# Kernel tuning notes

Measured on AMD Instinct MI355X. Metric: run time of the kernel, lower is better.

Reference implementation:

```python
import jax, jax.numpy as jnp
import numpy as np

B, H, W, C = 32, 112, 112, 96
HEADS, WS, SHIFT = 3, 7, 3
N = WS * WS            # tokens per window (49)
NW = (H // WS) * (W // WS)  # windows per image (256)
HD = C // HEADS


def _rel_pos_index():
    coords = np.stack(np.meshgrid(np.arange(WS), np.arange(WS), indexing='ij'))  # (2,ws,ws)
    cf = coords.reshape(2, -1)
    rel = (cf[:, :, None] - cf[:, None, :]).transpose(1, 2, 0)  # (N,N,2)
    rel[:, :, 0] += WS - 1
    rel[:, :, 1] += WS - 1
    rel[:, :, 0] *= 2 * WS - 1
    return jnp.asarray(rel.sum(-1))  # (N,N) int


def _attn_mask():
    img = np.zeros((H, W))
    sl = (slice(0, -WS), slice(-WS, -SHIFT), slice(-SHIFT, None))
    cnt = 0
    for hs in sl:
        for ws_ in sl:
            img[hs, ws_] = cnt
            cnt += 1
    mw = img.reshape(H // WS, WS, W // WS, WS).transpose(0, 2, 1, 3).reshape(-1, N)
    am = mw[:, None, :] - mw[:, :, None]
    return jnp.asarray(np.where(am != 0, -100.0, 0.0).astype(np.float32))  # (nW,N,N)


REL_IDX = _rel_pos_index()
ATTN_MASK = _attn_mask()


def _ln(x, w, b):
    m = x.mean(-1, keepdims=True)
    v = x.var(-1, keepdims=True)
    return (x - m) / jnp.sqrt(v + 1e-5) * w + b


def setup_inputs() -> dict:
    key = jax.random.key(0)
    ks = jax.random.split(key, 8)
    s = 0.02
    return {
        'x': jax.random.normal(ks[0], (B, H * W, C), jnp.float32),
        'norm1_w': jnp.ones((C,), jnp.float32),
        'norm1_b': jnp.zeros((C,), jnp.float32),
        'qkv_w': jax.random.normal(ks[1], (3 * C, C), jnp.float32) * s,
        'qkv_b': jnp.zeros((3 * C,), jnp.float32),
        'proj_w': jax.random.normal(ks[2], (C, C), jnp.float32) * s,
        'proj_b': jnp.zeros((C,), jnp.float32),
        'rpb_table': jax.random.normal(ks[3], ((2 * WS - 1) ** 2, HEADS), jnp.float32) * s,
        'norm2_w': jnp.ones((C,), jnp.float32),
        'norm2_b': jnp.zeros((C,), jnp.float32),
        'fc1_w': jax.random.normal(ks[4], (4 * C, C), jnp.float32) * s,
        'fc1_b': jnp.zeros((4 * C,), jnp.float32),
        'fc2_w': jax.random.normal(ks[5], (C, 4 * C), jnp.float32) * s,
        'fc2_b': jnp.zeros((C,), jnp.float32),
    }


def reference(x, norm1_w, norm1_b, qkv_w, qkv_b, proj_w, proj_b, rpb_table,
              norm2_w, norm2_b, fc1_w, fc1_b, fc2_w, fc2_b):
    shortcut = x
    xn = _ln(x, norm1_w, norm1_b).reshape(B, H, W, C)
    # cyclic shift
    xs = jnp.roll(xn, (-SHIFT, -SHIFT), axis=(1, 2))
    # window partition -> (B*nW, N, C)
    xw = xs.reshape(B, H // WS, WS, W // WS, WS, C).transpose(0, 1, 3, 2, 4, 5).reshape(B * NW, N, C)
    # windowed multi-head attention
    qkv = (xw @ qkv_w.T + qkv_b).reshape(B * NW, N, 3, HEADS, HD).transpose(2, 0, 3, 1, 4)
    q, k, v = qkv[0], qkv[1], qkv[2]
    attn = jnp.einsum('bhnd,bhmd->bhnm', q * (HD ** -0.5), k)
    bias = rpb_table[REL_IDX].transpose(2, 0, 1)  # (heads,N,N)
    attn = attn + bias[None]
    attn = attn.reshape(B, NW, HEADS, N, N) + ATTN_MASK[None, :, None]
    attn = jax.nn.softmax(attn.reshape(B * NW, HEADS, N, N), axis=-1)
    o = jnp.einsum('bhnm,bhmd->bhnd', attn, v).transpose(0, 2, 1, 3).reshape(B * NW, N, C)
    o = o @ proj_w.T + proj_b
    # window reverse + reverse shift
    xr = o.reshape(B, H // WS, W // WS, WS, WS, C).transpose(0, 1, 3, 2, 4, 5).reshape(B, H, W, C)
    xr = jnp.roll(xr, (SHIFT, SHIFT), axis=(1, 2)).reshape(B, H * W, C)
    # MLP (note: applied to norm2 of attention output, as in the source)
    xn2 = _ln(xr, norm2_w, norm2_b)
    h1 = jax.nn.gelu(xn2 @ fc1_w.T + fc1_b, approximate=False)
    mlp = h1 @ fc2_w.T + fc2_b
    return shortcut + xr + mlp
```

## Files before the change

### kernel.cpp

```cpp
#include <hip/hip_runtime.h>
#include <hip/hip_bf16.h>

#define NTOK 401408

typedef __attribute__((ext_vector_type(8))) short s8v;
typedef __attribute__((ext_vector_type(4))) float f4v;

__device__ __forceinline__ float bs2f(short s) {
  unsigned u = ((unsigned)(unsigned short)s) << 16;
  float f; __builtin_memcpy(&f, &u, 4); return f;
}
__device__ __forceinline__ short f2bs(float f) {
  __hip_bfloat16 b = __float2bfloat16(f);
  return *reinterpret_cast<short*>(&b);
}
__device__ __forceinline__ s8v ld8(const short* p) { return *(const s8v*)p; }
__device__ __forceinline__ int rgn(int a) { return (a < 105) ? 0 : ((a < 109) ? 1 : 2); }

__device__ __forceinline__ void wave_lds_fence() {
  asm volatile("s_waitcnt lgkmcnt(0)" ::: "memory");
  __builtin_amdgcn_sched_barrier(0);
}

__device__ __forceinline__ void ld8d(const void* base, size_t elem, int isb, float* o) {
  if (isb) {
    s8v v = *(const s8v*)((const short*)base + elem);
    #pragma unroll
    for (int j = 0; j < 8; j++) o[j] = bs2f(v[j]);
  } else {
    const float* f = (const float*)base + elem;
    float4 a = *(const float4*)f;
    float4 b = *(const float4*)(f + 4);
    o[0]=a.x; o[1]=a.y; o[2]=a.z; o[3]=a.w; o[4]=b.x; o[5]=b.y; o[6]=b.z; o[7]=b.w;
  }
}
__device__ __forceinline__ void st8d(void* base, size_t elem, int isb, const float* v) {
  if (isb) {
    s8v o;
    #pragma unroll
    for (int j = 0; j < 8; j++) o[j] = f2bs(v[j]);
    *(s8v*)((short*)base + elem) = o;
  } else {
    float* f = (float*)base + elem;
    float4 a = {v[0], v[1], v[2], v[3]};
    float4 b = {v[4], v[5], v[6], v[7]};
    *(float4*)f = a;
    *(float4*)(f + 4) = b;
  }
}
__device__ __forceinline__ float lddf(const void* base, size_t elem, int isb) {
  return isb ? bs2f(((const short*)base)[elem]) : ((const float*)base)[elem];
}
__device__ __forceinline__ void stdf(void* base, size_t elem, int isb, float v) {
  if (isb) ((short*)base)[elem] = f2bs(v); else ((float*)base)[elem] = v;
}

#define OQW   0
#define OQB   27648
#define OPW   27936
#define OPB   37152
#define ORPB  37248
#define ON1W  37760
#define ON1B  37856
#define ON2W  37952
#define ON2B  38048
#define OF1W  38144
#define OF1B  75008
#define OF2W  75392
#define OF2B  112256

__global__ __launch_bounds__(256) void k_detect_convert(
    const void* x,
    const void* qw, const void* qb, const void* pw, const void* pb, const void* rpb,
    const void* n1w, const void* n1b, const void* n2w, const void* n2b,
    const void* f1w, const void* f1b, const void* f2w, const void* f2b,
    int* flag, short* wb)
{
  __shared__ int cnt_sh;
  if (threadIdx.x == 0) cnt_sh = 0;
  __syncthreads();
  const unsigned* xw = (const unsigned*)x;
  int c = 0;
  for (int i = threadIdx.x; i < 1024; i += 256) {
    unsigned e = (xw[i] >> 7) & 0xFFu;
    if (e >= 0x70u && e <= 0x8Fu) c++;
  }
  atomicAdd(&cnt_sh, c);
  __syncthreads();
  const int isb = (cnt_sh > 512) ? 1 : 0;
  if (blockIdx.x == 0 && threadIdx.x == 0) *flag = isb;

  const void* srcs[13] = {qw, qb, pw, pb, rpb, n1w, n1b, n2w, n2b, f1w, f1b, f2w, f2b};
  const int   ns[13]   = {27648, 288, 9216, 96, 507, 96, 96, 96, 96, 36864, 384, 36864, 96};
  const int   offs[13] = {OQW, OQB, OPW, OPB, ORPB, ON1W, ON1B, ON2W, ON2B, OF1W, OF1B, OF2W, OF2B};
  const int gtid = blockIdx.x * 256 + threadIdx.x;
  for (int a = 0; a < 13; a++) {
    const void* s = srcs[a];
    for (int i = gtid; i < ns[a]; i += 64 * 256)
      wb[offs[a] + i] = f2bs(isb ? bs2f(((const short*)s)[i]) : ((const float*)s)[i]);
  }
}

__global__ __launch_bounds__(192, 3) void k_attn_fused(
    const void* __restrict__ xg, const short* __restrict__ wb,
    const int* __restrict__ flag, void* __restrict__ xrout)
{
  __shared__ __align__(16) short smem[22272];

  const int isb = *flag;
  const int h = threadIdx.x >> 6;
  const int lane = threadIdx.x & 63;
  const int quad = lane >> 4, l15 = lane & 15;
  const int wi = blockIdx.x;
  const int bb = wi >> 8, wp = wi & 255, wh = wp >> 4, ww = wp & 15;

  short* Qh = smem + h * 5120;
  short* Kh = Qh + 2560;
  short* Ph = smem + h * 5120;
  short* Vh = smem + 15360 + h * 2304;

  float gwv[3][8], gbv[3][8];
  #pragma unroll
  for (int kc = 0; kc < 3; kc++) {
    s8v g = ld8(wb + ON1W + kc * 32 + quad * 8);
    s8v t = ld8(wb + ON1B + kc * 32 + quad * 8);
    #pragma unroll
    for (int j = 0; j < 8; j++) { gwv[kc][j] = bs2f(g[j]); gbv[kc][j] = bs2f(t[j]); }
  }

  s8v af[4][3];
  #pragma unroll
  for (int rt = 0; rt < 4; rt++) {
    int n = rt * 16 + l15; if (n > 48) n = 48;
    int ii = n / 7, jj = n - ii * 7;
    int hi = wh * 7 + ii + 3; if (hi >= 112) hi -= 112;
    int wj = ww * 7 + jj + 3; if (wj >= 112) wj -= 112;
    size_t rowoff = ((size_t)bb * 12544 + hi * 112 + wj) * 96;
    float v[3][8]; float sm = 0.f, sq = 0.f;
    #pragma unroll
    for (int kc = 0; kc < 3; kc++) {
      ld8d(xg, rowoff + kc * 32 + quad * 8, isb, v[kc]);
      #pragma unroll
      for (int j = 0; j < 8; j++) { sm += v[kc][j]; sq += v[kc][j] * v[kc][j]; }
    }
    sm += __shfl_xor(sm, 16); sm += __shfl_xor(sm, 32);
    sq += __shfl_xor(sq, 16); sq += __shfl_xor(sq, 32);
    float mean = sm * (1.f / 96.f);
    float var  = sq * (1.f / 96.f) - mean * mean;
    float rstd = rsqrtf(var + 1e-5f);
    #pragma unroll
    for (int kc = 0; kc < 3; kc++) {
      s8v o;
      #pragma unroll
      for (int j = 0; j < 8; j++) o[j] = f2bs((v[kc][j] - mean) * rstd * gwv[kc][j] + gbv[kc][j]);
      af[rt][kc] = o;
    }
  }

  const float qscale = 0.1767766952966369f;
  #pragma unroll
  for (int s = 0; s < 3; s++) {
    #pragma unroll
    for (int nt = 0; nt < 2; nt++) {
      int col = s * 96 + h * 32 + nt * 16 + l15;
      const short* wrow = wb + OQW + (size_t)col * 96;
      s8v b0 = ld8(wrow + quad * 8), b1 = ld8(wrow + 32 + quad * 8), b2 = ld8(wrow + 64 + quad * 8);
      float bias = bs2f(wb[OQB + col]);
      #pragma unroll
      for (int rt = 0; rt < 4; rt++) {
        f4v acc = {0.f, 0.f, 0.f, 0.f};
        acc = __builtin_amdgcn_mfma_f32_16x16x32_bf16(af[rt][0], b0, acc, 0, 0, 0);
        acc = __builtin_amdgcn_mfma_f32_16x16x32_bf16(af[rt][1], b1, acc, 0, 0, 0);
        acc = __builtin_amdgcn_mfma_f32_16x16x32_bf16(af[rt][2], b2, acc, 0, 0, 0);
        #pragma unroll
        for (int r = 0; r < 4; r++) {
          int tok = rt * 16 + quad * 4 + r;
          float val = acc[r] + bias;
          int cc = nt * 16 + l15;
          if (s == 0)      Qh[tok * 40 + cc] = f2bs(val * qscale);
          else if (s == 1) Kh[tok * 40 + cc] = f2bs(val);
          else             Vh[cc * 72 + tok] = f2bs(val);
        }
      }
    }
  }
  wave_lds_fence();

  s8v qa[4], kb[4], vf[2][2];
  #pragma unroll
  for (int t = 0; t < 4; t++) {
    qa[t] = *(const s8v*)&Qh[(t * 16 + l15) * 40 + quad * 8];
    kb[t] = *(const s8v*)&Kh[(t * 16 + l15) * 40 + quad * 8];
  }
  #pragma unroll
  for (int nt = 0; nt < 2; nt++)
    #pragma unroll
    for (int kc = 0; kc < 2; kc++)
      vf[nt][kc] = *(const s8v*)&Vh[(nt * 16 + l15) * 72 + kc * 32 + quad * 8];

  int crid[4], ci[4], cj[4]; bool cv[4];
  #pragma unroll
  for (int nt = 0; nt < 4; nt++) {
    int col = nt * 16 + l15;
    cv[nt] = (col < 49);
    int ki = col / 7, kj = col - ki * 7;
    ci[nt] = ki; cj[nt] = kj;
    crid[nt] = rgn(wh * 7 + ki) * 3 + rgn(ww * 7 + kj);
  }

  #pragma unroll
  for (int rt = 0; rt < 4; rt++) {
    f4v sc4[4];
    #pragma unroll
    for (int nt = 0; nt < 4; nt++) {
      f4v z = {0.f, 0.f, 0.f, 0.f};
      sc4[nt] = __builtin_amdgcn_mfma_f32_16x16x32_bf16(qa[rt], kb[nt], z, 0, 0, 0);
    }
    #pragma unroll
    for (int rr = 0; rr < 4; rr++) {
      int row = rt * 16 + quad * 4 + rr;
      bool vr = (row < 49);
      int ri = row / 7, rj = row - ri * 7;
      int rrid = rgn(wh * 7 + ri) * 3 + rgn(ww * 7 + rj);
      float vals[4];
      float m = -1e30f;
      #pragma unroll
      for (int nt = 0; nt < 4; nt++) {
        float sv;
        if (vr && cv[nt]) {
          int bidx = (ri - ci[nt] + 6) * 13 + (rj - cj[nt] + 6);
          float bias = bs2f(wb[ORPB + bidx * 3 + h]);
          sv = sc4[nt][rr] + bias + ((rrid == crid[nt]) ? 0.f : -100.f);
        } else {
          sv = vr ? -1e30f : 0.f;
        }
        vals[nt] = sv;
        m = fmaxf(m, sv);
      }
      #pragma unroll
      for (int o = 1; o < 16; o <<= 1) m = fmaxf(m, __shfl_xor(m, o));
      float sum = 0.f;
      #pragma unroll
      for (int nt = 0; nt < 4; nt++) { vals[nt] = __expf(vals[nt] - m); sum += vals[nt]; }
      #pragma unroll
      for (int o = 1; o < 16; o <<= 1) sum += __shfl_xor(sum, o);
      float inv = 1.f / sum;
      #pragma unroll
      for (int nt = 0; nt < 4; nt++)
        Ph[row * 72 + nt * 16 + l15] = f2bs(vals[nt] * inv);
    }
  }
  wave_lds_fence();

  s8v pf[4][2];
  #pragma unroll
  for (int rt = 0; rt < 4; rt++)
    #pragma unroll
    for (int kc = 0; kc < 2; kc++)
      pf[rt][kc] = *(const s8v*)&Ph[(rt * 16 + l15) * 72 + kc * 32 + quad * 8];
  short* Oh = Vh;
  #pragma unroll
  for (int rt = 0; rt < 4; rt++) {
    #pragma unroll
    for (int nt = 0; nt < 2; nt++) {
      f4v acc = {0.f, 0.f, 0.f, 0.f};
      acc = __builtin_amdgcn_mfma_f32_16x16x32_bf16(pf[rt][0], vf[nt][0], acc, 0, 0, 0);
      acc = __builtin_amdgcn_mfma_f32_16x16x32_bf16(pf[rt][1], vf[nt][1], acc, 0, 0, 0);
      #pragma unroll
      for (int r = 0; r < 4; r++) {
        int tok = rt * 16 + quad * 4 + r;
        Oh[tok * 32 + nt * 16 + l15] = f2bs(acc[r]);
      }
    }
  }
  __syncthreads();

  s8v of[4][3];
  #pragma unroll
  for (int rt = 0; rt < 4; rt++)
    #pragma unroll
    for (int kc = 0; kc < 3; kc++)
      of[rt][kc] = *(const s8v*)&smem[15360 + kc * 2304 + (rt * 16 + l15) * 32 + quad * 8];
  #pragma unroll
  for (int nt = 0; nt < 2; nt++) {
    int col = h * 32 + nt * 16 + l15;
    const short* wrow = wb + OPW + (size_t)col * 96;
    s8v b0 = ld8(wrow + quad * 8), b1 = ld8(wrow + 32 + quad * 8), b2 = ld8(wrow + 64 + quad * 8);
    float bias = bs2f(wb[OPB + col]);
    #pragma unroll
    for (int rt = 0; rt < 4; rt++) {
      f4v acc = {0.f, 0.f, 0.f, 0.f};
      acc = __builtin_amdgcn_mfma_f32_16x16x32_bf16(of[rt][0], b0, acc, 0, 0, 0);
      acc = __builtin_amdgcn_mfma_f32_16x16x32_bf16(of[rt][1], b1, acc, 0, 0, 0);
      acc = __builtin_amdgcn_mfma_f32_16x16x32_bf16(of[rt][2], b2, acc, 0, 0, 0);
      #pragma unroll
      for (int r = 0; r < 4; r++) {
        int tok = rt * 16 + quad * 4 + r;
        if (tok < 49) {
          int ii = tok / 7, jj = tok - ii * 7;
          int hi = wh * 7 + ii + 3; if (hi >= 112) hi -= 112;
          int wj = ww * 7 + jj + 3; if (wj >= 112) wj -= 112;
          size_t dest = ((size_t)bb * 12544 + hi * 112 + wj) * 96 + col;
          stdf(xrout, dest, isb, acc[r] + bias);
        }
      }
    }
  }
}

__global__ __launch_bounds__(256, 3) void k_mlp(
    const void* xrv, const void* __restrict__ xg, const short* __restrict__ wb,
    const int* __restrict__ flag, void* outv)
{
  __shared__ __align__(16) short h_sh[4][16][392];

  const int isb = *flag;
  const int wave = threadIdx.x >> 6, lane = threadIdx.x & 63;
  const int quad = lane >> 4, l15 = lane & 15;
  const size_t m0 = (size_t)blockIdx.x * 256 + (size_t)wave * 64;

  s8v gw[3], gb[3];
  #pragma unroll
  for (int kc = 0; kc < 3; kc++) {
    gw[kc] = ld8(wb + ON2W + kc * 32 + quad * 8);
    gb[kc] = ld8(wb + ON2B + kc * 32 + quad * 8);
  }

  for (int rt = 0; rt < 4; rt++) {
    size_t ro = (m0 + rt * 16 + l15) * 96;
    float v[3][8]; float sm = 0.f, sq = 0.f;
    #pragma unroll
    for (int kc = 0; kc < 3; kc++) {
      ld8d(xrv, ro + kc * 32 + quad * 8, isb, v[kc]);
      #pragma unroll
      for (int j = 0; j < 8; j++) { sm += v[kc][j]; sq += v[kc][j] * v[kc][j]; }
    }
    sm += __shfl_xor(sm, 16); sm += __shfl_xor(sm, 32);
    sq += __shfl_xor(sq, 16); sq += __shfl_xor(sq, 32);
    float mean = sm * (1.f / 96.f);
    float var  = sq * (1.f / 96.f) - mean * mean;
    float rstd = rsqrtf(var + 1e-5f);
    s8v a2[3];
    #pragma unroll
    for (int kc = 0; kc < 3; kc++) {
      s8v o;
      #pragma unroll
      for (int j = 0; j < 8; j++)
        o[j] = f2bs((v[kc][j] - mean) * rstd * bs2f(gw[kc][j]) + bs2f(gb[kc][j]));
      a2[kc] = o;
    }

    for (int nt = 0; nt < 24; nt++) {
      int col = nt * 16 + l15;
      const short* wrow = wb + OF1W + (size_t)col * 96;
      s8v b0 = ld8(wrow + quad * 8), b1 = ld8(wrow + 32 + quad * 8), b2 = ld8(wrow + 64 + quad * 8);
      float bias = bs2f(wb[OF1B + col]);
      f4v acc = {0.f, 0.f, 0.f, 0.f};
      acc = __builtin_amdgcn_mfma_f32_16x16x32_bf16(a2[0], b0, acc, 0, 0, 0);
      acc = __builtin_amdgcn_mfma_f32_16x16x32_bf16(a2[1], b1, acc, 0, 0, 0);
      acc = __builtin_amdgcn_mfma_f32_16x16x32_bf16(a2[2], b2, acc, 0, 0, 0);
      #pragma unroll
      for (int r = 0; r < 4; r++) {
        float hv = acc[r] + bias;
        hv = 0.5f * hv * (1.f + erff(hv * 0.7071067811865475f));
        h_sh[wave][quad * 4 + r][col] = f2bs(hv);
      }
    }
    wave_lds_fence();

    f4v acc6[6];
    #pragma unroll
    for (int nt = 0; nt < 6; nt++) { f4v z = {0.f, 0.f, 0.f, 0.f}; acc6[nt] = z; }
    for (int kc = 0; kc < 12; kc++) {
      s8v ha = *(const s8v*)&h_sh[wave][l15][kc * 32 + quad * 8];
      #pragma unroll
      for (int nt = 0; nt < 6; nt++) {
        s8v b = ld8(wb + OF2W + (size_t)(nt * 16 + l15) * 384 + kc * 32 + quad * 8);
        acc6[nt] = __builtin_amdgcn_mfma_f32_16x16x32_bf16(ha, b, acc6[nt], 0, 0, 0);
      }
    }

    float* ot = (float*)&h_sh[wave][0][0];
    #pragma unroll
    for (int nt = 0; nt < 6; nt++) {
      float bias = bs2f(wb[OF2B + nt * 16 + l15]);
      #pragma unroll
      for (int r = 0; r < 4; r++)
        ot[(quad * 4 + r) * 100 + nt * 16 + l15] = acc6[nt][r] + bias;
    }
    wave_lds_fence();

    size_t grow = m0 + rt * 16 + l15;
    #pragma unroll
    for (int j = 0; j < 3; j++) {
      int c0 = (quad + 4 * j) * 8;
      float vx[8], vr[8], vo[8];
      ld8d(xg,  grow * 96 + c0, isb, vx);
      ld8d(xrv, grow * 96 + c0, isb, vr);
      #pragma unroll
      for (int e = 0; e < 8; e++) vo[e] = ot[l15 * 100 + c0 + e] + vx[e] + vr[e];
      st8d(outv, grow * 96 + c0, isb, vo);
    }
  }
}

extern "C" void kernel_launch(void* const* d_in, const int* in_sizes, int n_in,
                              void* d_out, int out_size, void* d_ws, size_t ws_size,
                              hipStream_t stream) {
  int*   flag = (int*)d_ws;
  short* wb   = (short*)d_ws + 8;

  k_detect_convert<<<64, 256, 0, stream>>>(
      d_in[0],
      d_in[3], d_in[4], d_in[5], d_in[6], d_in[7],
      d_in[1], d_in[2], d_in[8], d_in[9],
      d_in[10], d_in[11], d_in[12], d_in[13],
      flag, wb);
  k_attn_fused<<<32 * 256, 192, 0, stream>>>(d_in[0], wb, flag, d_out);
  k_mlp<<<NTOK / 256, 256, 0, stream>>>(d_out, d_in[0], wb, flag, d_out);
}
```

Baseline: 1.067 ms.

## Split attention rows across two waves per head, chunk MLP hidden, use tanh GELU

The attention kernel now launches 384 threads, so two waves share each head and each handles half of the row tiles. This needs block-wide syncs around the shared Q/K/V reads. The MLP kernel processes the hidden dimension in two halves, which halves the LDS scratch and raises the occupancy target. Exact erf GELU is replaced by a tanh approximation computed with exp, which is cheaper but deviates slightly from the exact GELU the reference uses.

```diff
diff --git a/kernel.cpp b/kernel.cpp
--- a/kernel.cpp
+++ b/kernel.cpp
@@ -20,6 +20,13 @@
 __device__ __forceinline__ void wave_lds_fence() {
   asm volatile("s_waitcnt lgkmcnt(0)" ::: "memory");
   __builtin_amdgcn_sched_barrier(0);
+}
+
+__device__ __forceinline__ float gelu_f(float x) {
+  float y = 1.5957691216057308f * x * (1.f + 0.044715f * x * x);
+  float t = __expf(y);
+  float th = 1.f - 2.f / (1.f + t);
+  return 0.5f * x * (1.f + th);
 }
 
 __device__ __forceinline__ void ld8d(const void* base, size_t elem, int isb, float* o) {
@@ -101,14 +108,16 @@
   }
 }
 
-__global__ __launch_bounds__(192, 3) void k_attn_fused(
+__global__ __launch_bounds__(384, 5) void k_attn_fused(
     const void* __restrict__ xg, const short* __restrict__ wb,
     const int* __restrict__ flag, void* __restrict__ xrout)
 {
   __shared__ __align__(16) short smem[22272];
 
   const int isb = *flag;
-  const int h = threadIdx.x >> 6;
+  const int wave = threadIdx.x >> 6;
+  const int h = (wave >= 3) ? wave - 3 : wave;
+  const int rtb = (wave >= 3) ? 2 : 0;
   const int lane = threadIdx.x & 63;
   const int quad = lane >> 4, l15 = lane & 15;
   const int wi = blockIdx.x;
@@ -119,19 +128,17 @@
   short* Ph = smem + h * 5120;
   short* Vh = smem + 15360 + h * 2304;
 
-  float gwv[3][8], gbv[3][8];
+  s8v gw1[3], gb1[3];
   #pragma unroll
   for (int kc = 0; kc < 3; kc++) {
-    s8v g = ld8(wb + ON1W + kc * 32 + quad * 8);
-    s8v t = ld8(wb + ON1B + kc * 32 + quad * 8);
-    #pragma unroll
-    for (int j = 0; j < 8; j++) { gwv[kc][j] = bs2f(g[j]); gbv[kc][j] = bs2f(t[j]); }
-  }
-
-  s8v af[4][3];
-  #pragma unroll
-  for (int rt = 0; rt < 4; rt++) {
-    int n = rt * 16 + l15; if (n > 48) n = 48;
+    gw1[kc] = ld8(wb + ON1W + kc * 32 + quad * 8);
+    gb1[kc] = ld8(wb + ON1B + kc * 32 + quad * 8);
+  }
+
+  s8v af[2][3];
+  #pragma unroll
+  for (int t = 0; t < 2; t++) {
+    int n = (rtb + t) * 16 + l15; if (n > 48) n = 48;
     int ii = n / 7, jj = n - ii * 7;
     int hi = wh * 7 + ii + 3; if (hi >= 112) hi -= 112;
     int wj = ww * 7 + jj + 3; if (wj >= 112) wj -= 112;
@@ -152,8 +159,9 @@
     for (int kc = 0; kc < 3; kc++) {
       s8v o;
       #pragma unroll
-      for (int j = 0; j < 8; j++) o[j] = f2bs((v[kc][j] - mean) * rstd * gwv[kc][j] + gbv[kc][j]);
-      af[rt][kc] = o;
+      for (int j = 0; j < 8; j++)
+        o[j] = f2bs((v[kc][j] - mean) * rstd * bs2f(gw1[kc][j]) + bs2f(gb1[kc][j]));
+      af[t][kc] = o;
     }
   }
 
@@ -167,14 +175,14 @@
       s8v b0 = ld8(wrow + quad * 8), b1 = ld8(wrow + 32 + quad * 8), b2 = ld8(wrow + 64 + quad * 8);
       float bias = bs2f(wb[OQB + col]);
       #pragma unroll
-      for (int rt = 0; rt < 4; rt++) {
+      for (int t = 0; t < 2; t++) {
         f4v acc = {0.f, 0.f, 0.f, 0.f};
-        acc = __builtin_amdgcn_mfma_f32_16x16x32_bf16(af[rt][0], b0, acc, 0, 0, 0);
-        acc = __builtin_amdgcn_mfma_f32_16x16x32_bf16(af[rt][1], b1, acc, 0, 0, 0);
-        acc = __builtin_amdgcn_mfma_f32_16x16x32_bf16(af[rt][2], b2, acc, 0, 0, 0);
+        acc = __builtin_amdgcn_mfma_f32_16x16x32_bf16(af[t][0], b0, acc, 0, 0, 0);
+        acc = __builtin_amdgcn_mfma_f32_16x16x32_bf16(af[t][1], b1, acc, 0, 0, 0);
+        acc = __builtin_amdgcn_mfma_f32_16x16x32_bf16(af[t][2], b2, acc, 0, 0, 0);
         #pragma unroll
         for (int r = 0; r < 4; r++) {
-          int tok = rt * 16 + quad * 4 + r;
+          int tok = (rtb + t) * 16 + quad * 4 + r;
           float val = acc[r] + bias;
           int cc = nt * 16 + l15;
           if (s == 0)      Qh[tok * 40 + cc] = f2bs(val * qscale);
@@ -184,19 +192,21 @@
       }
     }
   }
-  wave_lds_fence();
-
-  s8v qa[4], kb[4], vf[2][2];
-  #pragma unroll
-  for (int t = 0; t < 4; t++) {
-    qa[t] = *(const s8v*)&Qh[(t * 16 + l15) * 40 + quad * 8];
-    kb[t] = *(const s8v*)&Kh[(t * 16 + l15) * 40 + quad * 8];
-  }
+  __syncthreads();
+
+  s8v qa[2], kb[4], vf[2][2];
+  #pragma unroll
+  for (int t = 0; t < 2; t++)
+    qa[t] = *(const s8v*)&Qh[((rtb + t) * 16 + l15) * 40 + quad * 8];
+  #pragma unroll
+  for (int nt = 0; nt < 4; nt++)
+    kb[nt] = *(const s8v*)&Kh[(nt * 16 + l15) * 40 + quad * 8];
   #pragma unroll
   for (int nt = 0; nt < 2; nt++)
     #pragma unroll
     for (int kc = 0; kc < 2; kc++)
       vf[nt][kc] = *(const s8v*)&Vh[(nt * 16 + l15) * 72 + kc * 32 + quad * 8];
+  __syncthreads();
 
   int crid[4], ci[4], cj[4]; bool cv[4];
   #pragma unroll
@@ -209,16 +219,16 @@
   }
 
   #pragma unroll
-  for (int rt = 0; rt < 4; rt++) {
+  for (int t = 0; t < 2; t++) {
     f4v sc4[4];
     #pragma unroll
     for (int nt = 0; nt < 4; nt++) {
       f4v z = {0.f, 0.f, 0.f, 0.f};
-      sc4[nt] = __builtin_amdgcn_mfma_f32_16x16x32_bf16(qa[rt], kb[nt], z, 0, 0, 0);
+      sc4[nt] = __builtin_amdgcn_mfma_f32_16x16x32_bf16(qa[t], kb[nt], z, 0, 0, 0);
     }
     #pragma unroll
     for (int rr = 0; rr < 4; rr++) {
-      int row = rt * 16 + quad * 4 + rr;
+      int row = (rtb + t) * 16 + quad * 4 + rr;
       bool vr = (row < 49);
       int ri = row / 7, rj = row - ri * 7;
       int rrid = rgn(wh * 7 + ri) * 3 + rgn(ww * 7 + rj);
@@ -252,35 +262,35 @@
   }
   wave_lds_fence();
 
-  s8v pf[4][2];
-  #pragma unroll
-  for (int rt = 0; rt < 4; rt++)
+  s8v pf[2][2];
+  #pragma unroll
+  for (int t = 0; t < 2; t++)
     #pragma unroll
     for (int kc = 0; kc < 2; kc++)
-      pf[rt][kc] = *(const s8v*)&Ph[(rt * 16 + l15) * 72 + kc * 32 + quad * 8];
+      pf[t][kc] = *(const s8v*)&Ph[((rtb + t) * 16 + l15) * 72 + kc * 32 + quad * 8];
   short* Oh = Vh;
   #pragma unroll
-  for (int rt = 0; rt < 4; rt++) {
+  for (int t = 0; t < 2; t++) {
     #pragma unroll
     for (int nt = 0; nt < 2; nt++) {
       f4v acc = {0.f, 0.f, 0.f, 0.f};
-      acc = __builtin_amdgcn_mfma_f32_16x16x32_bf16(pf[rt][0], vf[nt][0], acc, 0, 0, 0);
-      acc = __builtin_amdgcn_mfma_f32_16x16x32_bf16(pf[rt][1], vf[nt][1], acc, 0, 0, 0);
+      acc = __builtin_amdgcn_mfma_f32_16x16x32_bf16(pf[t][0], vf[nt][0], acc, 0, 0, 0);
+      acc = __builtin_amdgcn_mfma_f32_16x16x32_bf16(pf[t][1], vf[nt][1], acc, 0, 0, 0);
       #pragma unroll
       for (int r = 0; r < 4; r++) {
-        int tok = rt * 16 + quad * 4 + r;
+        int tok = (rtb + t) * 16 + quad * 4 + r;
         Oh[tok * 32 + nt * 16 + l15] = f2bs(acc[r]);
       }
     }
   }
   __syncthreads();
 
-  s8v of[4][3];
-  #pragma unroll
-  for (int rt = 0; rt < 4; rt++)
+  s8v of[2][3];
+  #pragma unroll
+  for (int t = 0; t < 2; t++)
     #pragma unroll
     for (int kc = 0; kc < 3; kc++)
-      of[rt][kc] = *(const s8v*)&smem[15360 + kc * 2304 + (rt * 16 + l15) * 32 + quad * 8];
+      of[t][kc] = *(const s8v*)&smem[15360 + kc * 2304 + ((rtb + t) * 16 + l15) * 32 + quad * 8];
   #pragma unroll
   for (int nt = 0; nt < 2; nt++) {
     int col = h * 32 + nt * 16 + l15;
@@ -288,14 +298,14 @@
     s8v b0 = ld8(wrow + quad * 8), b1 = ld8(wrow + 32 + quad * 8), b2 = ld8(wrow + 64 + quad * 8);
     float bias = bs2f(wb[OPB + col]);
     #pragma unroll
-    for (int rt = 0; rt < 4; rt++) {
+    for (int t = 0; t < 2; t++) {
       f4v acc = {0.f, 0.f, 0.f, 0.f};
-      acc = __builtin_amdgcn_mfma_f32_16x16x32_bf16(of[rt][0], b0, acc, 0, 0, 0);
-      acc = __builtin_amdgcn_mfma_f32_16x16x32_bf16(of[rt][1], b1, acc, 0, 0, 0);
-      acc = __builtin_amdgcn_mfma_f32_16x16x32_bf16(of[rt][2], b2, acc, 0, 0, 0);
+      acc = __builtin_amdgcn_mfma_f32_16x16x32_bf16(of[t][0], b0, acc, 0, 0, 0);
+      acc = __builtin_amdgcn_mfma_f32_16x16x32_bf16(of[t][1], b1, acc, 0, 0, 0);
+      acc = __builtin_amdgcn_mfma_f32_16x16x32_bf16(of[t][2], b2, acc, 0, 0, 0);
       #pragma unroll
       for (int r = 0; r < 4; r++) {
-        int tok = rt * 16 + quad * 4 + r;
+        int tok = (rtb + t) * 16 + quad * 4 + r;
         if (tok < 49) {
           int ii = tok / 7, jj = tok - ii * 7;
           int hi = wh * 7 + ii + 3; if (hi >= 112) hi -= 112;
@@ -308,11 +318,11 @@
   }
 }
 
-__global__ __launch_bounds__(256, 3) void k_mlp(
+__global__ __launch_bounds__(256, 6) void k_mlp(
     const void* xrv, const void* __restrict__ xg, const short* __restrict__ wb,
     const int* __restrict__ flag, void* outv)
 {
-  __shared__ __align__(16) short h_sh[4][16][392];
+  __shared__ __align__(16) short h_sh[4][16][200];
 
   const int isb = *flag;
   const int wave = threadIdx.x >> 6, lane = threadIdx.x & 63;
@@ -350,34 +360,35 @@
       a2[kc] = o;
     }
 
-    for (int nt = 0; nt < 24; nt++) {
-      int col = nt * 16 + l15;
-      const short* wrow = wb + OF1W + (size_t)col * 96;
-      s8v b0 = ld8(wrow + quad * 8), b1 = ld8(wrow + 32 + quad * 8), b2 = ld8(wrow + 64 + quad * 8);
-      float bias = bs2f(wb[OF1B + col]);
-      f4v acc = {0.f, 0.f, 0.f, 0.f};
-      acc = __builtin_amdgcn_mfma_f32_16x16x32_bf16(a2[0], b0, acc, 0, 0, 0);
-      acc = __builtin_amdgcn_mfma_f32_16x16x32_bf16(a2[1], b1, acc, 0, 0, 0);
-      acc = __builtin_amdgcn_mfma_f32_16x16x32_bf16(a2[2], b2, acc, 0, 0, 0);
-      #pragma unroll
-      for (int r = 0; r < 4; r++) {
-        float hv = acc[r] + bias;
-        hv = 0.5f * hv * (1.f + erff(hv * 0.7071067811865475f));
-        h_sh[wave][quad * 4 + r][col] = f2bs(hv);
-      }
-    }
-    wave_lds_fence();
-
     f4v acc6[6];
     #pragma unroll
     for (int nt = 0; nt < 6; nt++) { f4v z = {0.f, 0.f, 0.f, 0.f}; acc6[nt] = z; }
-    for (int kc = 0; kc < 12; kc++) {
-      s8v ha = *(const s8v*)&h_sh[wave][l15][kc * 32 + quad * 8];
-      #pragma unroll
-      for (int nt = 0; nt < 6; nt++) {
-        s8v b = ld8(wb + OF2W + (size_t)(nt * 16 + l15) * 384 + kc * 32 + quad * 8);
-        acc6[nt] = __builtin_amdgcn_mfma_f32_16x16x32_bf16(ha, b, acc6[nt], 0, 0, 0);
-      }
+
+    for (int half = 0; half < 2; half++) {
+      for (int nt = 0; nt < 12; nt++) {
+        int col = half * 192 + nt * 16 + l15;
+        const short* wrow = wb + OF1W + (size_t)col * 96;
+        s8v b0 = ld8(wrow + quad * 8), b1 = ld8(wrow + 32 + quad * 8), b2 = ld8(wrow + 64 + quad * 8);
+        float bias = bs2f(wb[OF1B + col]);
+        f4v acc = {0.f, 0.f, 0.f, 0.f};
+        acc = __builtin_amdgcn_mfma_f32_16x16x32_bf16(a2[0], b0, acc, 0, 0, 0);
+        acc = __builtin_amdgcn_mfma_f32_16x16x32_bf16(a2[1], b1, acc, 0, 0, 0);
+        acc = __builtin_amdgcn_mfma_f32_16x16x32_bf16(a2[2], b2, acc, 0, 0, 0);
+        #pragma unroll
+        for (int r = 0; r < 4; r++)
+          h_sh[wave][quad * 4 + r][nt * 16 + l15] = f2bs(gelu_f(acc[r] + bias));
+      }
+      wave_lds_fence();
+
+      for (int kc = 0; kc < 6; kc++) {
+        s8v ha = *(const s8v*)&h_sh[wave][l15][kc * 32 + quad * 8];
+        #pragma unroll
+        for (int nt = 0; nt < 6; nt++) {
+          s8v b = ld8(wb + OF2W + (size_t)(nt * 16 + l15) * 384 + half * 192 + kc * 32 + quad * 8);
+          acc6[nt] = __builtin_amdgcn_mfma_f32_16x16x32_bf16(ha, b, acc6[nt], 0, 0, 0);
+        }
+      }
+      wave_lds_fence();
     }
 
     float* ot = (float*)&h_sh[wave][0][0];
@@ -401,6 +412,7 @@
       for (int e = 0; e < 8; e++) vo[e] = ot[l15 * 100 + c0 + e] + vx[e] + vr[e];
       st8d(outv, grow * 96 + c0, isb, vo);
     }
+    wave_lds_fence();
   }
 }
 
@@ -416,6 +428,6 @@
       d_in[1], d_in[2], d_in[8], d_in[9],
       d_in[10], d_in[11], d_in[12], d_in[13],
       flag, wb);
-  k_attn_fused<<<32 * 256, 192, 0, stream>>>(d_in[0], wb, flag, d_out);
+  k_attn_fused<<<32 * 256, 384, 0, stream>>>(d_in[0], wb, flag, d_out);
   k_mlp<<<NTOK / 256, 256, 0, stream>>>(d_out, d_in[0], wb, flag, d_out);
 }
```

After: 1.215 ms. 13.9% more time.
